# Kernel optimization log

Hardware: AMD Instinct MI355X
Metric: run time of the kernel (lower is better)

Reference implementation:

```python
import jax, jax.numpy as jnp
import numpy as np


def setup_inputs() -> dict:
    key = jax.random.key(0)
    k1, k2, k3, k4, k5 = jax.random.split(key, 5)
    B, C, H, W = 32, 256, 64, 64
    R = 16  # reduction -> hidden = C // R = 16
    hid = C // R
    return {
        "x": jax.random.normal(k1, (B, C, H, W), dtype=jnp.float32),
        "w1": jax.random.normal(k2, (hid, 1, 1, 1), dtype=jnp.float32) * 0.1,
        "b1": jax.random.normal(k3, (hid,), dtype=jnp.float32) * 0.1,
        "w2": jax.random.normal(k4, (C, hid, 1, 1), dtype=jnp.float32) * 0.1,
        "b2": jax.random.normal(k5, (C,), dtype=jnp.float32) * 0.1,
    }


def reference(x, w1, b1, w2, b2):
    # PositionalAveragePooling: mean over channel dim -> [B, 1, H, W]
    s = jnp.mean(x, axis=1)  # [B, H, W]
    # conv1 (1 -> hid, 1x1): per-position scalar times weight vector + bias
    w1v = w1[:, 0, 0, 0]  # [hid]
    h = jax.nn.relu(s[:, None, :, :] * w1v[None, :, None, None]
                    + b1[None, :, None, None])  # [B, hid, H, W]
    # conv2 (hid -> C, 1x1): pointwise matmul over channel dim
    w2m = w2[:, :, 0, 0]  # [C, hid]
    scale = jax.nn.sigmoid(jnp.einsum("bkhw,ck->bchw", h, w2m)
                           + b2[None, :, None, None])  # [B, C, H, W]
    return x * scale
```

## Files before the change

### kernel.cpp

```cpp
#include <hip/hip_runtime.h>

#define NB 32
#define NC 256
#define NH 64
#define NW 64
#define NK 16
#define HW (NH * NW)
#define NIT 8
#define NBLK (NB * NH / NIT)

typedef float f32x4 __attribute__((ext_vector_type(4)));

__device__ __forceinline__ float fsig(float z) {
    return __builtin_amdgcn_rcpf(1.0f + __expf(-z));
}

__global__ __launch_bounds__(1024, 4) void pse_kernel(
    const float* __restrict__ x,
    const float* __restrict__ w1,
    const float* __restrict__ b1,
    const float* __restrict__ w2,
    const float* __restrict__ b2,
    float* __restrict__ out)
{
    __shared__ float w2t[NK][NC + 4];
    __shared__ f32x4 part[16][17];
    __shared__ f32x4 hv4[NK][16];
    __shared__ float b2s[NC];

    const int t   = threadIdx.x;
    const int cg  = t >> 4;
    const int q   = t & 15;
    const int wid = t >> 6;
    const int blk = blockIdx.x;

    {
        const f32x4 v = reinterpret_cast<const f32x4*>(w2)[t];
        const int c  = t >> 2;
        const int k0 = (t & 3) << 2;
        w2t[k0 + 0][c] = v.x; w2t[k0 + 1][c] = v.y;
        w2t[k0 + 2][c] = v.z; w2t[k0 + 3][c] = v.w;
        if (t < NC) b2s[t] = b2[t];
    }
    float w1k = 0.f, b1k = 0.f;
    if (t < 256) { const int k = t >> 4; w1k = w1[k]; b1k = b1[k]; }

    const size_t lane_off = (size_t)(cg << 2) * HW + (q << 2);

    f32x4 xv[2][4];

#define ROWPTR(IT, BASE) \
    ((BASE) + (size_t)((((IT) << 8) + blk) >> 6) * NC * HW \
            + (size_t)((((IT) << 8) + blk) & 63) * NW + lane_off)

#define LOADROW(BUF, IT) { \
    const float* _p = ROWPTR(IT, x); \
    _Pragma("unroll") \
    for (int _i = 0; _i < 4; ++_i) \
        BUF[_i] = __builtin_nontemporal_load( \
            reinterpret_cast<const f32x4*>(_p + (size_t)_i * HW)); }

    LOADROW(xv[0], 0)

    #pragma unroll
    for (int it = 0; it < NIT; ++it) {
        const int cur = it & 1, nxt = cur ^ 1;

        if (it + 1 < NIT) LOADROW(xv[nxt], it + 1)

        {
            f32x4 p = xv[cur][0] + xv[cur][1] + xv[cur][2] + xv[cur][3];
            p.x += __shfl_xor(p.x, 16, 64); p.y += __shfl_xor(p.y, 16, 64);
            p.z += __shfl_xor(p.z, 16, 64); p.w += __shfl_xor(p.w, 16, 64);
            p.x += __shfl_xor(p.x, 32, 64); p.y += __shfl_xor(p.y, 32, 64);
            p.z += __shfl_xor(p.z, 32, 64); p.w += __shfl_xor(p.w, 32, 64);
            if ((t & 63) < 16) part[wid][q] = p;
        }
        __syncthreads();

        if (t < 256) {
            f32x4 s = (f32x4)(0.f);
            #pragma unroll
            for (int i = 0; i < 16; ++i) s += part[i][q];
            s *= (1.0f / (float)NC);
            f32x4 hv;
            hv.x = fmaxf(fmaf(s.x, w1k, b1k), 0.f);
            hv.y = fmaxf(fmaf(s.y, w1k, b1k), 0.f);
            hv.z = fmaxf(fmaf(s.z, w1k, b1k), 0.f);
            hv.w = fmaxf(fmaf(s.w, w1k, b1k), 0.f);
            hv4[t >> 4][q] = hv;
        }
        __syncthreads();

        {
            f32x4 acc0 = (f32x4)(b2s[(cg << 2) + 0]);
            f32x4 acc1 = (f32x4)(b2s[(cg << 2) + 1]);
            f32x4 acc2 = (f32x4)(b2s[(cg << 2) + 2]);
            f32x4 acc3 = (f32x4)(b2s[(cg << 2) + 3]);
            #pragma unroll
            for (int k = 0; k < NK; ++k) {
                const f32x4 hk = hv4[k][q];
                const f32x4 wvv = *reinterpret_cast<const f32x4*>(&w2t[k][cg << 2]);
                acc0 += hk * wvv.x; acc1 += hk * wvv.y;
                acc2 += hk * wvv.z; acc3 += hk * wvv.w;
            }
            float* _o = const_cast<float*>(ROWPTR(it, out));
            const f32x4 xc0 = xv[cur][0], xc1 = xv[cur][1];
            const f32x4 xc2 = xv[cur][2], xc3 = xv[cur][3];
            f32x4 r;
            r.x = xc0.x * fsig(acc0.x); r.y = xc0.y * fsig(acc0.y);
            r.z = xc0.z * fsig(acc0.z); r.w = xc0.w * fsig(acc0.w);
            __builtin_nontemporal_store(r, reinterpret_cast<f32x4*>(_o + 0 * (size_t)HW));
            r.x = xc1.x * fsig(acc1.x); r.y = xc1.y * fsig(acc1.y);
            r.z = xc1.z * fsig(acc1.z); r.w = xc1.w * fsig(acc1.w);
            __builtin_nontemporal_store(r, reinterpret_cast<f32x4*>(_o + 1 * (size_t)HW));
            r.x = xc2.x * fsig(acc2.x); r.y = xc2.y * fsig(acc2.y);
            r.z = xc2.z * fsig(acc2.z); r.w = xc2.w * fsig(acc2.w);
            __builtin_nontemporal_store(r, reinterpret_cast<f32x4*>(_o + 2 * (size_t)HW));
            r.x = xc3.x * fsig(acc3.x); r.y = xc3.y * fsig(acc3.y);
            r.z = xc3.z * fsig(acc3.z); r.w = xc3.w * fsig(acc3.w);
            __builtin_nontemporal_store(r, reinterpret_cast<f32x4*>(_o + 3 * (size_t)HW));
        }
    }
#undef LOADROW
#undef ROWPTR
}

extern "C" void kernel_launch(void* const* d_in, const int* in_sizes, int n_in,
                              void* d_out, int out_size, void* d_ws, size_t ws_size,
                              hipStream_t stream) {
    const float* x  = (const float*)d_in[0];
    const float* w1 = (const float*)d_in[1];
    const float* b1 = (const float*)d_in[2];
    const float* w2 = (const float*)d_in[3];
    const float* b2 = (const float*)d_in[4];
    float* out = (float*)d_out;

    hipLaunchKernelGGL(pse_kernel, dim3(NBLK), dim3(1024), 0, stream,
                       x, w1, b1, w2, b2, out);
}
```

Baseline: 234.6 us.

## Assign contiguous rows per block, halve rows per block, raise occupancy hint

Each block now handles a contiguous run of NIT rows of one image, where before its rows were strided 256 apart across the grid, so address math becomes a simple base pointer plus offsets. NIT drops from 8 to 4, doubling the block count, and the launch-bounds minimum rises to 8 blocks per CU. The first row load is issued before the weight staging into shared memory so it overlaps that setup. Shorter per-block loops cost more weight-staging overhead per row, and the stronger launch bound tightens register pressure.

```diff
diff --git a/kernel.cpp b/kernel.cpp
--- a/kernel.cpp
+++ b/kernel.cpp
@@ -6,7 +6,7 @@
 #define NW 64
 #define NK 16
 #define HW (NH * NW)
-#define NIT 8
+#define NIT 4
 #define NBLK (NB * NH / NIT)
 
 typedef float f32x4 __attribute__((ext_vector_type(4)));
@@ -15,7 +15,7 @@
     return __builtin_amdgcn_rcpf(1.0f + __expf(-z));
 }
 
-__global__ __launch_bounds__(1024, 4) void pse_kernel(
+__global__ __launch_bounds__(1024, 8) void pse_kernel(
     const float* __restrict__ x,
     const float* __restrict__ w1,
     const float* __restrict__ b1,
@@ -32,7 +32,25 @@
     const int cg  = t >> 4;
     const int q   = t & 15;
     const int wid = t >> 6;
-    const int blk = blockIdx.x;
+
+    const int bh0 = blockIdx.x * NIT;
+    const int b   = bh0 >> 6;
+    const int h0  = bh0 & 63;
+
+    const size_t base = (size_t)b * NC * HW + (size_t)h0 * NW
+                      + (size_t)(cg << 2) * HW + (q << 2);
+    const float* __restrict__ xb = x + base;
+    float* __restrict__ ob       = out + base;
+
+    f32x4 xv[2][4];
+
+#define LOADROW(BUF, IT) { \
+    _Pragma("unroll") \
+    for (int _i = 0; _i < 4; ++_i) \
+        BUF[_i] = __builtin_nontemporal_load( \
+            reinterpret_cast<const f32x4*>(xb + (IT) * NW + _i * HW)); }
+
+    LOADROW(xv[0], 0)
 
     {
         const f32x4 v = reinterpret_cast<const f32x4*>(w2)[t];
@@ -44,23 +62,6 @@
     }
     float w1k = 0.f, b1k = 0.f;
     if (t < 256) { const int k = t >> 4; w1k = w1[k]; b1k = b1[k]; }
-
-    const size_t lane_off = (size_t)(cg << 2) * HW + (q << 2);
-
-    f32x4 xv[2][4];
-
-#define ROWPTR(IT, BASE) \
-    ((BASE) + (size_t)((((IT) << 8) + blk) >> 6) * NC * HW \
-            + (size_t)((((IT) << 8) + blk) & 63) * NW + lane_off)
-
-#define LOADROW(BUF, IT) { \
-    const float* _p = ROWPTR(IT, x); \
-    _Pragma("unroll") \
-    for (int _i = 0; _i < 4; ++_i) \
-        BUF[_i] = __builtin_nontemporal_load( \
-            reinterpret_cast<const f32x4*>(_p + (size_t)_i * HW)); }
-
-    LOADROW(xv[0], 0)
 
     #pragma unroll
     for (int it = 0; it < NIT; ++it) {
@@ -99,31 +100,28 @@
             f32x4 acc3 = (f32x4)(b2s[(cg << 2) + 3]);
             #pragma unroll
             for (int k = 0; k < NK; ++k) {
-                const f32x4 hk = hv4[k][q];
+                const f32x4 hk  = hv4[k][q];
                 const f32x4 wvv = *reinterpret_cast<const f32x4*>(&w2t[k][cg << 2]);
                 acc0 += hk * wvv.x; acc1 += hk * wvv.y;
                 acc2 += hk * wvv.z; acc3 += hk * wvv.w;
             }
-            float* _o = const_cast<float*>(ROWPTR(it, out));
-            const f32x4 xc0 = xv[cur][0], xc1 = xv[cur][1];
-            const f32x4 xc2 = xv[cur][2], xc3 = xv[cur][3];
+            float* _o = ob + it * NW;
             f32x4 r;
-            r.x = xc0.x * fsig(acc0.x); r.y = xc0.y * fsig(acc0.y);
-            r.z = xc0.z * fsig(acc0.z); r.w = xc0.w * fsig(acc0.w);
-            __builtin_nontemporal_store(r, reinterpret_cast<f32x4*>(_o + 0 * (size_t)HW));
-            r.x = xc1.x * fsig(acc1.x); r.y = xc1.y * fsig(acc1.y);
-            r.z = xc1.z * fsig(acc1.z); r.w = xc1.w * fsig(acc1.w);
-            __builtin_nontemporal_store(r, reinterpret_cast<f32x4*>(_o + 1 * (size_t)HW));
-            r.x = xc2.x * fsig(acc2.x); r.y = xc2.y * fsig(acc2.y);
-            r.z = xc2.z * fsig(acc2.z); r.w = xc2.w * fsig(acc2.w);
-            __builtin_nontemporal_store(r, reinterpret_cast<f32x4*>(_o + 2 * (size_t)HW));
-            r.x = xc3.x * fsig(acc3.x); r.y = xc3.y * fsig(acc3.y);
-            r.z = xc3.z * fsig(acc3.z); r.w = xc3.w * fsig(acc3.w);
-            __builtin_nontemporal_store(r, reinterpret_cast<f32x4*>(_o + 3 * (size_t)HW));
+            r.x = xv[cur][0].x * fsig(acc0.x); r.y = xv[cur][0].y * fsig(acc0.y);
+            r.z = xv[cur][0].z * fsig(acc0.z); r.w = xv[cur][0].w * fsig(acc0.w);
+            __builtin_nontemporal_store(r, reinterpret_cast<f32x4*>(_o + 0 * HW));
+            r.x = xv[cur][1].x * fsig(acc1.x); r.y = xv[cur][1].y * fsig(acc1.y);
+            r.z = xv[cur][1].z * fsig(acc1.z); r.w = xv[cur][1].w * fsig(acc1.w);
+            __builtin_nontemporal_store(r, reinterpret_cast<f32x4*>(_o + 1 * HW));
+            r.x = xv[cur][2].x * fsig(acc2.x); r.y = xv[cur][2].y * fsig(acc2.y);
+            r.z = xv[cur][2].z * fsig(acc2.z); r.w = xv[cur][2].w * fsig(acc2.w);
+            __builtin_nontemporal_store(r, reinterpret_cast<f32x4*>(_o + 2 * HW));
+            r.x = xv[cur][3].x * fsig(acc3.x); r.y = xv[cur][3].y * fsig(acc3.y);
+            r.z = xv[cur][3].z * fsig(acc3.z); r.w = xv[cur][3].w * fsig(acc3.w);
+            __builtin_nontemporal_store(r, reinterpret_cast<f32x4*>(_o + 3 * HW));
         }
     }
 #undef LOADROW
-#undef ROWPTR
 }
 
 extern "C" void kernel_launch(void* const* d_in, const int* in_sizes, int n_in,
```

After: 252.6 us. 7.6% more time.
